# Performance work log

Measured on AMD Instinct MI355X. Metric: run time of the kernel, lower is better.

The kernel has to match this reference:

```python
import jax, jax.numpy as jnp
import numpy as np

EPS = 1e-8


def _cdist(a, b):
    # a: [B,N,3], b: [B,M,3] -> euclidean distances [B,N,M]
    a2 = jnp.sum(a * a, axis=-1)[:, :, None]          # [B,N,1]
    b2 = jnp.sum(b * b, axis=-1)[:, None, :]          # [B,1,M]
    ab = jnp.einsum('bnd,bmd->bnm', a, b)             # [B,N,M]
    d2 = jnp.maximum(a2 + b2 - 2.0 * ab, 0.0)
    return jnp.sqrt(d2)


def setup_inputs() -> dict:
    key = jax.random.key(0)
    ks = jax.random.split(key, 8)
    B, N, M, C1, C2 = 16, 4096, 1024, 128, 256
    Cin = C1 + C2  # 384
    H1, H2 = 256, 128
    return {
        'xyz1': jax.random.normal(ks[0], (B, N, 3), dtype=jnp.float32),
        'xyz2': jax.random.normal(ks[1], (B, M, 3), dtype=jnp.float32),
        'points1': jax.random.normal(ks[2], (B, C1, N), dtype=jnp.float32),
        'points2': jax.random.normal(ks[3], (B, C2, M), dtype=jnp.float32),
        'W1': jax.random.normal(ks[4], (H1, Cin), dtype=jnp.float32) * (1.0 / np.sqrt(Cin)),
        'b1': jnp.zeros((H1,), dtype=jnp.float32),
        'W2': jax.random.normal(ks[5], (H2, H1), dtype=jnp.float32) * (1.0 / np.sqrt(H1)),
        'b2': jnp.zeros((H2,), dtype=jnp.float32),
    }


def reference(xyz1, xyz2, points1, points2, W1, b1, W2, b2):
    # inverse-distance weighted interpolation over ALL M source points
    dist = _cdist(xyz1, xyz2) + EPS                   # [B,N,M]
    inv = 1.0 / dist
    weight = inv / jnp.sum(inv, axis=-1, keepdims=True)
    # interpolated features: [B,N,M] @ [B,M,C2] -> [B,C2,N]
    interpolated = jnp.einsum('bnm,bcm->bcn', weight, points2)
    new_points = jnp.concatenate([points1, interpolated], axis=1)  # [B,C1+C2,N]
    # 1x1 Conv1d MLP with ReLU
    h = jax.nn.relu(jnp.einsum('oc,bcn->bon', W1, new_points) + b1[None, :, None])
    out = jax.nn.relu(jnp.einsum('oc,bcn->bon', W2, h) + b2[None, :, None])
    return out
```

## Files before the change

kernel.cpp:

```cpp
#include <hip/hip_runtime.h>
#include <math.h>

#define BBATCH 16
#define NPTS   4096
#define MPTS   1024
#define C1c    128
#define C2c    256
#define CINc   384
#define H1c    256
#define H2c    128
#define TN     64

typedef _Float16 f16x8 __attribute__((ext_vector_type(8)));
typedef _Float16 f16x4 __attribute__((ext_vector_type(4)));
typedef float    f32x4 __attribute__((ext_vector_type(4)));

#define LDIW 136
#define LDXc 408
#define LDH  264

#define OFF_XYZ2  0
#define OFF_INV   12288
#define OFF_RED   47104
#define OFF_RECIP 52224
#define SMEM_BYTES 52480

#define NFRAG_P2  (BBATCH * 32 * 16 * 64)
#define NFRAG_W1  (16 * 12 * 64)
#define NFRAG_W2  (8 * 8 * 64)
#define WS_P2S  0
#define WS_W1S  (NFRAG_P2 * 8)
#define WS_W2S  (WS_W1S + NFRAG_W1 * 8)
#define WS_F16_TOTAL (WS_W2S + NFRAG_W2 * 8)

__global__ __launch_bounds__(256) void cvt_swz(
    const float* __restrict__ p2, const float* __restrict__ W1,
    const float* __restrict__ W2, _Float16* __restrict__ ws)
{
    const int t = blockIdx.x * 256 + threadIdx.x;
    const float* src;
    _Float16* dst;
    if (t < NFRAG_P2) {
        const int lane = t & 63, wt = (t >> 6) & 15, s = (t >> 10) & 31, b = t >> 15;
        const int c = wt * 16 + (lane & 15);
        const int m = s * 32 + (lane >> 4) * 8;
        src = p2 + ((size_t)(b * C2c + c)) * MPTS + m;
        dst = ws + WS_P2S + (size_t)t * 8;
    } else if (t < NFRAG_P2 + NFRAG_W1) {
        const int u = t - NFRAG_P2;
        const int lane = u & 63, kc = (u >> 6) % 12, wt = (u >> 6) / 12;
        const int o = wt * 16 + (lane & 15);
        const int k = kc * 32 + (lane >> 4) * 8;
        src = W1 + (size_t)o * CINc + k;
        dst = ws + WS_W1S + (size_t)u * 8;
    } else {
        const int v = t - NFRAG_P2 - NFRAG_W1;
        const int lane = v & 63, oc = (v >> 6) & 7, wt2 = v >> 9;
        const int o = wt2 * 16 + (lane & 15);
        const int k = oc * 32 + (lane >> 4) * 8;
        src = W2 + (size_t)o * H1c + k;
        dst = ws + WS_W2S + (size_t)v * 8;
    }
    const float4 a0 = *(const float4*)(src);
    const float4 a1 = *(const float4*)(src + 4);
    f16x8 h;
    h[0] = (_Float16)a0.x; h[1] = (_Float16)a0.y; h[2] = (_Float16)a0.z; h[3] = (_Float16)a0.w;
    h[4] = (_Float16)a1.x; h[5] = (_Float16)a1.y; h[6] = (_Float16)a1.z; h[7] = (_Float16)a1.w;
    *(f16x8*)dst = h;
}

template <bool F16P>
__global__ __launch_bounds__(256, 3) void fp_mfma7(
    const float* __restrict__ xyz1, const float* __restrict__ xyz2,
    const float* __restrict__ p1,   const float* __restrict__ p2,
    const float* __restrict__ W1,   const float* __restrict__ b1v,
    const float* __restrict__ W2,   const float* __restrict__ b2v,
    const _Float16* __restrict__ p2s, const _Float16* __restrict__ W1s,
    const _Float16* __restrict__ W2s,
    float* __restrict__ out)
{
    __shared__ __align__(16) char smem[SMEM_BYTES];
    float*    s_xyz2  = (float*)(smem + OFF_XYZ2);
    _Float16* s_inv   = (_Float16*)(smem + OFF_INV);
    float*    s_red   = (float*)(smem + OFF_RED);
    float*    s_recip = (float*)(smem + OFF_RECIP);
    _Float16* s_X     = (_Float16*)smem;
    _Float16* s_H     = (_Float16*)smem;

    const int tid  = threadIdx.x;
    const int w    = tid >> 6;
    const int L    = tid & 63;
    const int quad = L >> 4;
    const int l16  = L & 15;

    const int id = blockIdx.x;
    const int b  = (id & 7) * 2 + ((id >> 3) & 1);
    const int n0 = (id >> 4) * TN;

    const float* __restrict__ z2b = xyz2 + (size_t)b * MPTS * 3;
    const float* __restrict__ p2b = p2   + (size_t)b * C2c * MPTS;
    const _Float16* __restrict__ p2sb =
        F16P ? (p2s + (((size_t)b * 32 * 16 + (size_t)w * 4) * 64 + L) * 8) : (const _Float16*)nullptr;

    for (int i = tid; i < MPTS * 3 / 4; i += 256)
        ((f32x4*)s_xyz2)[i] = ((const f32x4*)z2b)[i];

    const float x1x = xyz1[((size_t)b * NPTS + n0 + L) * 3 + 0];
    const float x1y = xyz1[((size_t)b * NPTS + n0 + L) * 3 + 1];
    const float x1z = xyz1[((size_t)b * NPTS + n0 + L) * 3 + 2];

    f32x4 acc[4][4];
    #pragma unroll
    for (int ct = 0; ct < 4; ++ct)
        #pragma unroll
        for (int nt = 0; nt < 4; ++nt)
            acc[ct][nt] = (f32x4){0.f, 0.f, 0.f, 0.f};

    float ssum = 0.f;
    f16x8 Aa[2][4];

    auto loadA = [&](int s, f16x8 dst[4]) {
        if (F16P) {
            const _Float16* ap = p2sb + (size_t)s * (16 * 64 * 8);
            #pragma unroll
            for (int ct = 0; ct < 4; ++ct)
                dst[ct] = *(const f16x8*)(ap + (size_t)ct * (64 * 8));
        } else {
            const float* ap = p2b + (size_t)(w * 64 + l16) * MPTS + s * 32 + quad * 8;
            #pragma unroll
            for (int ct = 0; ct < 4; ++ct) {
                const float4 a0 = *(const float4*)(ap + (size_t)ct * (16 * MPTS));
                const float4 a1 = *(const float4*)(ap + (size_t)ct * (16 * MPTS) + 4);
                f16x8 h;
                h[0] = (_Float16)a0.x; h[1] = (_Float16)a0.y; h[2] = (_Float16)a0.z; h[3] = (_Float16)a0.w;
                h[4] = (_Float16)a1.x; h[5] = (_Float16)a1.y; h[6] = (_Float16)a1.z; h[7] = (_Float16)a1.w;
                dst[ct] = h;
            }
        }
    };

    auto gen = [&](int ss_) {
        _Float16* buf = s_inv + (ss_ & 1) * (64 * LDIW);
        #pragma unroll
        for (int g = 0; g < 4; ++g) {
            const float* zp = s_xyz2 + (size_t)(ss_ * 128 + w * 32 + g * 8) * 3;
            f32x4 zr[6];
            #pragma unroll
            for (int j = 0; j < 6; ++j) zr[j] = ((const f32x4*)zp)[j];
            const float* zv = (const float*)zr;
            f16x8 iv;
            #pragma unroll
            for (int i = 0; i < 8; ++i) {
                const float dx = x1x - zv[3 * i + 0];
                const float dy = x1y - zv[3 * i + 1];
                const float dz = x1z - zv[3 * i + 2];
                const float d2 = fmaf(dx, dx, fmaf(dy, dy, fmaf(dz, dz, 1e-12f)));
                const float inv = __builtin_amdgcn_rsqf(d2);
                ssum += inv;
                iv[i] = (_Float16)inv;
            }
            *(f16x8*)(buf + L * LDIW + w * 32 + g * 8) = iv;
        }
    };

    __syncthreads();
    loadA(0, Aa[0]);
    gen(0);
    __syncthreads();

    for (int ss = 0; ss < 8; ++ss) {
        if (ss + 1 < 8) gen(ss + 1);
        const _Float16* buf = s_inv + (ss & 1) * (64 * LDIW);
        #pragma unroll
        for (int cc = 0; cc < 4; ++cc) {
            const int s = ss * 4 + cc;
            if (s + 1 < 32) loadA(s + 1, Aa[(cc + 1) & 1]);
            const _Float16* bb = buf + l16 * LDIW + cc * 32 + quad * 8;
            #pragma unroll
            for (int nt = 0; nt < 4; ++nt) {
                const f16x8 bf = *(const f16x8*)(bb + nt * (16 * LDIW));
                #pragma unroll
                for (int ct = 0; ct < 4; ++ct)
                    acc[ct][nt] = __builtin_amdgcn_mfma_f32_16x16x32_f16(Aa[cc & 1][ct], bf, acc[ct][nt], 0, 0, 0);
            }
        }
        __syncthreads();
    }

    s_red[tid] = ssum;
    __syncthreads();
    if (tid < 64)
        s_recip[tid] = 1.0f / (s_red[tid] + s_red[tid + 64] + s_red[tid + 128] + s_red[tid + 192]);
    __syncthreads();

    {
        float rn4[4];
        #pragma unroll
        for (int nt = 0; nt < 4; ++nt) rn4[nt] = s_recip[nt * 16 + l16];
        #pragma unroll
        for (int ct = 0; ct < 4; ++ct)
            #pragma unroll
            for (int nt = 0; nt < 4; ++nt) {
                const f32x4 v = acc[ct][nt];
                const float r = rn4[nt];
                f16x4 hv;
                hv[0] = (_Float16)(v[0] * r);
                hv[1] = (_Float16)(v[1] * r);
                hv[2] = (_Float16)(v[2] * r);
                hv[3] = (_Float16)(v[3] * r);
                *(f16x4*)(&s_X[(nt * 16 + l16) * LDXc + 128 + w * 64 + ct * 16 + quad * 4]) = hv;
            }
    }
    {
        const float* p1b = p1 + (size_t)b * C1c * NPTS + n0;
        #pragma unroll
        for (int cc = 0; cc < 8; ++cc) {
            const int c = w * 32 + cc * 4;
            f16x4 v;
            v[0] = (_Float16)p1b[(size_t)(c + 0) * NPTS + L];
            v[1] = (_Float16)p1b[(size_t)(c + 1) * NPTS + L];
            v[2] = (_Float16)p1b[(size_t)(c + 2) * NPTS + L];
            v[3] = (_Float16)p1b[(size_t)(c + 3) * NPTS + L];
            *(f16x4*)(&s_X[L * LDXc + c]) = v;
        }
    }
    __syncthreads();

    f32x4 hacc[4][4];
    #pragma unroll
    for (int ct = 0; ct < 4; ++ct)
        #pragma unroll
        for (int nt = 0; nt < 4; ++nt)
            hacc[ct][nt] = (f32x4){0.f, 0.f, 0.f, 0.f};

    #pragma unroll 2
    for (int kc = 0; kc < 12; ++kc) {
        f16x8 af[4];
        if (F16P) {
            const _Float16* wp = W1s + (((size_t)(w * 4) * 12 + kc) * 64 + L) * 8;
            #pragma unroll
            for (int ct = 0; ct < 4; ++ct)
                af[ct] = *(const f16x8*)(wp + (size_t)ct * (12 * 64 * 8));
        } else {
            const float* wp = W1 + (size_t)(w * 64 + l16) * CINc + kc * 32 + quad * 8;
            #pragma unroll
            for (int ct = 0; ct < 4; ++ct) {
                const float4 a0 = *(const float4*)(wp + ct * (16 * CINc));
                const float4 a1 = *(const float4*)(wp + ct * (16 * CINc) + 4);
                f16x8 h;
                h[0] = (_Float16)a0.x; h[1] = (_Float16)a0.y; h[2] = (_Float16)a0.z; h[3] = (_Float16)a0.w;
                h[4] = (_Float16)a1.x; h[5] = (_Float16)a1.y; h[6] = (_Float16)a1.z; h[7] = (_Float16)a1.w;
                af[ct] = h;
            }
        }
        #pragma unroll
        for (int nt = 0; nt < 4; ++nt) {
            const f16x8 bf = *(const f16x8*)(&s_X[(nt * 16 + l16) * LDXc + kc * 32 + quad * 8]);
            #pragma unroll
            for (int ct = 0; ct < 4; ++ct)
                hacc[ct][nt] = __builtin_amdgcn_mfma_f32_16x16x32_f16(af[ct], bf, hacc[ct][nt], 0, 0, 0);
        }
    }

    __syncthreads();

    {
        f32x4 bb[4];
        #pragma unroll
        for (int ct = 0; ct < 4; ++ct)
            bb[ct] = *(const f32x4*)(b1v + w * 64 + ct * 16 + quad * 4);
        #pragma unroll
        for (int ct = 0; ct < 4; ++ct)
            #pragma unroll
            for (int nt = 0; nt < 4; ++nt) {
                const f32x4 v = hacc[ct][nt];
                f16x4 hv;
                hv[0] = (_Float16)fmaxf(v[0] + bb[ct][0], 0.f);
                hv[1] = (_Float16)fmaxf(v[1] + bb[ct][1], 0.f);
                hv[2] = (_Float16)fmaxf(v[2] + bb[ct][2], 0.f);
                hv[3] = (_Float16)fmaxf(v[3] + bb[ct][3], 0.f);
                *(f16x4*)(&s_H[(nt * 16 + l16) * LDH + w * 64 + ct * 16 + quad * 4]) = hv;
            }
    }
    __syncthreads();

    f32x4 oacc[2][4];
    #pragma unroll
    for (int ct = 0; ct < 2; ++ct)
        #pragma unroll
        for (int nt = 0; nt < 4; ++nt)
            oacc[ct][nt] = (f32x4){0.f, 0.f, 0.f, 0.f};

    #pragma unroll 2
    for (int oc = 0; oc < 8; ++oc) {
        f16x8 af2[2];
        if (F16P) {
            const _Float16* wp = W2s + (((size_t)(w * 2) * 8 + oc) * 64 + L) * 8;
            #pragma unroll
            for (int ct = 0; ct < 2; ++ct)
                af2[ct] = *(const f16x8*)(wp + (size_t)ct * (8 * 64 * 8));
        } else {
            const float* wp = W2 + (size_t)(w * 32 + l16) * H1c + oc * 32 + quad * 8;
            #pragma unroll
            for (int ct = 0; ct < 2; ++ct) {
                const float4 a0 = *(const float4*)(wp + ct * (16 * H1c));
                const float4 a1 = *(const float4*)(wp + ct * (16 * H1c) + 4);
                f16x8 h;
                h[0] = (_Float16)a0.x; h[1] = (_Float16)a0.y; h[2] = (_Float16)a0.z; h[3] = (_Float16)a0.w;
                h[4] = (_Float16)a1.x; h[5] = (_Float16)a1.y; h[6] = (_Float16)a1.z; h[7] = (_Float16)a1.w;
                af2[ct] = h;
            }
        }
        #pragma unroll
        for (int nt = 0; nt < 4; ++nt) {
            const f16x8 bf = *(const f16x8*)(&s_H[(nt * 16 + l16) * LDH + oc * 32 + quad * 8]);
            #pragma unroll
            for (int ct = 0; ct < 2; ++ct)
                oacc[ct][nt] = __builtin_amdgcn_mfma_f32_16x16x32_f16(af2[ct], bf, oacc[ct][nt], 0, 0, 0);
        }
    }

    {
        f32x4 bb2[2];
        #pragma unroll
        for (int ct = 0; ct < 2; ++ct)
            bb2[ct] = *(const f32x4*)(b2v + w * 32 + ct * 16 + quad * 4);
        #pragma unroll
        for (int ct = 0; ct < 2; ++ct)
            #pragma unroll
            for (int nt = 0; nt < 4; ++nt) {
                float* op = out + ((size_t)b * H2c + w * 32 + ct * 16 + quad * 4) * NPTS
                                + n0 + nt * 16 + l16;
                #pragma unroll
                for (int j = 0; j < 4; ++j)
                    op[(size_t)j * NPTS] = fmaxf(oacc[ct][nt][j] + bb2[ct][j], 0.f);
            }
    }
}

extern "C" void kernel_launch(void* const* d_in, const int* in_sizes, int n_in,
                              void* d_out, int out_size, void* d_ws, size_t ws_size,
                              hipStream_t stream) {
    (void)in_sizes; (void)n_in; (void)out_size;
    const float* xyz1 = (const float*)d_in[0];
    const float* xyz2 = (const float*)d_in[1];
    const float* p1   = (const float*)d_in[2];
    const float* p2   = (const float*)d_in[3];
    const float* W1   = (const float*)d_in[4];
    const float* b1   = (const float*)d_in[5];
    const float* W2   = (const float*)d_in[6];
    const float* b2   = (const float*)d_in[7];
    float* out = (float*)d_out;

    dim3 grid(BBATCH * (NPTS / TN));
    dim3 block(256);
    if (ws_size >= (size_t)WS_F16_TOTAL * 2) {
        _Float16* ws = (_Float16*)d_ws;
        const int nswz = NFRAG_P2 + NFRAG_W1 + NFRAG_W2;
        cvt_swz<<<dim3(nswz / 256), dim3(256), 0, stream>>>(p2, W1, W2, ws);
        fp_mfma7<true><<<grid, block, 0, stream>>>(xyz1, xyz2, p1, p2, W1, b1, W2, b2,
                                                   ws + WS_P2S, ws + WS_W1S, ws + WS_W2S, out);
    } else {
        fp_mfma7<false><<<grid, block, 0, stream>>>(xyz1, xyz2, p1, p2, W1, b1, W2, b2,
                                                    nullptr, nullptr, nullptr, out);
    }
}
```

Measured before the change: 171.7 us.

## Shrink LDS footprint with fragment-swizzled layouts and stream points1 directly into MFMA

Drops the shared-memory copy of xyz2 and reads it from global or L1 inside the generator. The inverse-distance, X and H buffers switch from padded row-major to MFMA-fragment-ordered layouts, so a single 32KB union plus a small reduction area replaces the 52KB allocation. points1 is no longer staged in LDS; its first four K-chunks are loaded from global and fed straight into MFMAs, and launch bounds are raised from 3 to 4 blocks per SM. The goal is higher occupancy and fewer LDS bank conflicts, at the cost of repeated global reads of xyz2 and strided uncoalesced-ish points1 loads inside the MLP.

```diff
diff --git a/kernel.cpp b/kernel.cpp
--- a/kernel.cpp
+++ b/kernel.cpp
@@ -15,15 +15,9 @@
 typedef _Float16 f16x4 __attribute__((ext_vector_type(4)));
 typedef float    f32x4 __attribute__((ext_vector_type(4)));
 
-#define LDIW 136
-#define LDXc 408
-#define LDH  264
-
-#define OFF_XYZ2  0
-#define OFF_INV   12288
-#define OFF_RED   47104
-#define OFF_RECIP 52224
-#define SMEM_BYTES 52480
+#define INV_HALF   8192
+#define SMEM_UNION 32768
+#define SMEM_BYTES (SMEM_UNION + 1024)
 
 #define NFRAG_P2  (BBATCH * 32 * 16 * 64)
 #define NFRAG_W1  (16 * 12 * 64)
@@ -70,7 +64,7 @@
 }
 
 template <bool F16P>
-__global__ __launch_bounds__(256, 3) void fp_mfma7(
+__global__ __launch_bounds__(256, 4) void fp_mfma8(
     const float* __restrict__ xyz1, const float* __restrict__ xyz2,
     const float* __restrict__ p1,   const float* __restrict__ p2,
     const float* __restrict__ W1,   const float* __restrict__ b1v,
@@ -80,12 +74,10 @@
     float* __restrict__ out)
 {
     __shared__ __align__(16) char smem[SMEM_BYTES];
-    float*    s_xyz2  = (float*)(smem + OFF_XYZ2);
-    _Float16* s_inv   = (_Float16*)(smem + OFF_INV);
-    float*    s_red   = (float*)(smem + OFF_RED);
-    float*    s_recip = (float*)(smem + OFF_RECIP);
-    _Float16* s_X     = (_Float16*)smem;
-    _Float16* s_H     = (_Float16*)smem;
+    _Float16* s_inv = (_Float16*)smem;
+    _Float16* s_X   = (_Float16*)smem;
+    _Float16* s_H   = (_Float16*)smem;
+    float*    s_red = (float*)(smem + SMEM_UNION);
 
     const int tid  = threadIdx.x;
     const int w    = tid >> 6;
@@ -101,9 +93,6 @@
     const float* __restrict__ p2b = p2   + (size_t)b * C2c * MPTS;
     const _Float16* __restrict__ p2sb =
         F16P ? (p2s + (((size_t)b * 32 * 16 + (size_t)w * 4) * 64 + L) * 8) : (const _Float16*)nullptr;
-
-    for (int i = tid; i < MPTS * 3 / 4; i += 256)
-        ((f32x4*)s_xyz2)[i] = ((const f32x4*)z2b)[i];
 
     const float x1x = xyz1[((size_t)b * NPTS + n0 + L) * 3 + 0];
     const float x1y = xyz1[((size_t)b * NPTS + n0 + L) * 3 + 1];
@@ -140,10 +129,11 @@
     };
 
     auto gen = [&](int ss_) {
-        _Float16* buf = s_inv + (ss_ & 1) * (64 * LDIW);
+        _Float16* buf = s_inv + (ss_ & 1) * INV_HALF;
+        const float* zbase = z2b + (size_t)(ss_ * 128 + w * 32) * 3;
         #pragma unroll
         for (int g = 0; g < 4; ++g) {
-            const float* zp = s_xyz2 + (size_t)(ss_ * 128 + w * 32 + g * 8) * 3;
+            const float* zp = zbase + g * 24;
             f32x4 zr[6];
             #pragma unroll
             for (int j = 0; j < 6; ++j) zr[j] = ((const f32x4*)zp)[j];
@@ -159,26 +149,24 @@
                 ssum += inv;
                 iv[i] = (_Float16)inv;
             }
-            *(f16x8*)(buf + L * LDIW + w * 32 + g * 8) = iv;
+            *(f16x8*)(buf + (((w * 4 + quad) * 64) + g * 16 + l16) * 8) = iv;
         }
     };
 
-    __syncthreads();
     loadA(0, Aa[0]);
     gen(0);
     __syncthreads();
 
     for (int ss = 0; ss < 8; ++ss) {
         if (ss + 1 < 8) gen(ss + 1);
-        const _Float16* buf = s_inv + (ss & 1) * (64 * LDIW);
+        const _Float16* buf = s_inv + (ss & 1) * INV_HALF;
         #pragma unroll
         for (int cc = 0; cc < 4; ++cc) {
             const int s = ss * 4 + cc;
             if (s + 1 < 32) loadA(s + 1, Aa[(cc + 1) & 1]);
-            const _Float16* bb = buf + l16 * LDIW + cc * 32 + quad * 8;
-            #pragma unroll
-            for (int nt = 0; nt < 4; ++nt) {
-                const f16x8 bf = *(const f16x8*)(bb + nt * (16 * LDIW));
+            #pragma unroll
+            for (int nt = 0; nt < 4; ++nt) {
+                const f16x8 bf = *(const f16x8*)(buf + ((cc * 4 + nt) * 64 + L) * 8);
                 #pragma unroll
                 for (int ct = 0; ct < 4; ++ct)
                     acc[ct][nt] = __builtin_amdgcn_mfma_f32_16x16x32_f16(Aa[cc & 1][ct], bf, acc[ct][nt], 0, 0, 0);
@@ -190,15 +178,18 @@
     s_red[tid] = ssum;
     __syncthreads();
     if (tid < 64)
-        s_recip[tid] = 1.0f / (s_red[tid] + s_red[tid + 64] + s_red[tid + 128] + s_red[tid + 192]);
+        s_red[tid] = 1.0f / (s_red[tid] + s_red[tid + 64] + s_red[tid + 128] + s_red[tid + 192]);
     __syncthreads();
 
     {
         float rn4[4];
         #pragma unroll
-        for (int nt = 0; nt < 4; ++nt) rn4[nt] = s_recip[nt * 16 + l16];
-        #pragma unroll
-        for (int ct = 0; ct < 4; ++ct)
+        for (int nt = 0; nt < 4; ++nt) rn4[nt] = s_red[nt * 16 + l16];
+        #pragma unroll
+        for (int ct = 0; ct < 4; ++ct) {
+            const int kq = 2 * w + (ct >> 1);
+            const int lp = l16 + 16 * (((ct & 1) * 2) + (quad >> 1));
+            const int jo = (quad & 1) * 4;
             #pragma unroll
             for (int nt = 0; nt < 4; ++nt) {
                 const f32x4 v = acc[ct][nt];
@@ -208,20 +199,8 @@
                 hv[1] = (_Float16)(v[1] * r);
                 hv[2] = (_Float16)(v[2] * r);
                 hv[3] = (_Float16)(v[3] * r);
-                *(f16x4*)(&s_X[(nt * 16 + l16) * LDXc + 128 + w * 64 + ct * 16 + quad * 4]) = hv;
-            }
-    }
-    {
-        const float* p1b = p1 + (size_t)b * C1c * NPTS + n0;
-        #pragma unroll
-        for (int cc = 0; cc < 8; ++cc) {
-            const int c = w * 32 + cc * 4;
-            f16x4 v;
-            v[0] = (_Float16)p1b[(size_t)(c + 0) * NPTS + L];
-            v[1] = (_Float16)p1b[(size_t)(c + 1) * NPTS + L];
-            v[2] = (_Float16)p1b[(size_t)(c + 2) * NPTS + L];
-            v[3] = (_Float16)p1b[(size_t)(c + 3) * NPTS + L];
-            *(f16x4*)(&s_X[L * LDXc + c]) = v;
+                *(f16x4*)(s_X + ((kq * 4 + nt) * 64 + lp) * 8 + jo) = hv;
+            }
         }
     }
     __syncthreads();
@@ -233,8 +212,46 @@
         for (int nt = 0; nt < 4; ++nt)
             hacc[ct][nt] = (f32x4){0.f, 0.f, 0.f, 0.f};
 
+    {
+        const float* p1f = p1 + ((size_t)b * C1c + quad * 8) * NPTS + n0 + l16;
+        #pragma unroll
+        for (int kc = 0; kc < 4; ++kc) {
+            f16x8 af[4];
+            if (F16P) {
+                const _Float16* wp = W1s + (((size_t)(w * 4) * 12 + kc) * 64 + L) * 8;
+                #pragma unroll
+                for (int ct = 0; ct < 4; ++ct)
+                    af[ct] = *(const f16x8*)(wp + (size_t)ct * (12 * 64 * 8));
+            } else {
+                const float* wp = W1 + (size_t)(w * 64 + l16) * CINc + kc * 32 + quad * 8;
+                #pragma unroll
+                for (int ct = 0; ct < 4; ++ct) {
+                    const float4 a0 = *(const float4*)(wp + ct * (16 * CINc));
+                    const float4 a1 = *(const float4*)(wp + ct * (16 * CINc) + 4);
+                    f16x8 h;
+                    h[0] = (_Float16)a0.x; h[1] = (_Float16)a0.y; h[2] = (_Float16)a0.z; h[3] = (_Float16)a0.w;
+                    h[4] = (_Float16)a1.x; h[5] = (_Float16)a1.y; h[6] = (_Float16)a1.z; h[7] = (_Float16)a1.w;
+                    af[ct] = h;
+                }
+            }
+            #pragma unroll
+            for (int nt = 0; nt < 4; ++nt) {
+                const float* pp = p1f + (size_t)(kc * 32) * NPTS + nt * 16;
+                float t[8];
+                #pragma unroll
+                for (int j = 0; j < 8; ++j) t[j] = pp[(size_t)j * NPTS];
+                f16x8 bf;
+                #pragma unroll
+                for (int j = 0; j < 8; ++j) bf[j] = (_Float16)t[j];
+                #pragma unroll
+                for (int ct = 0; ct < 4; ++ct)
+                    hacc[ct][nt] = __builtin_amdgcn_mfma_f32_16x16x32_f16(af[ct], bf, hacc[ct][nt], 0, 0, 0);
+            }
+        }
+    }
+
     #pragma unroll 2
-    for (int kc = 0; kc < 12; ++kc) {
+    for (int kc = 4; kc < 12; ++kc) {
         f16x8 af[4];
         if (F16P) {
             const _Float16* wp = W1s + (((size_t)(w * 4) * 12 + kc) * 64 + L) * 8;
@@ -255,7 +272,7 @@
         }
         #pragma unroll
         for (int nt = 0; nt < 4; ++nt) {
-            const f16x8 bf = *(const f16x8*)(&s_X[(nt * 16 + l16) * LDXc + kc * 32 + quad * 8]);
+            const f16x8 bf = *(const f16x8*)(s_X + (((kc - 4) * 4 + nt) * 64 + L) * 8);
             #pragma unroll
             for (int ct = 0; ct < 4; ++ct)
                 hacc[ct][nt] = __builtin_amdgcn_mfma_f32_16x16x32_f16(af[ct], bf, hacc[ct][nt], 0, 0, 0);
@@ -270,7 +287,10 @@
         for (int ct = 0; ct < 4; ++ct)
             bb[ct] = *(const f32x4*)(b1v + w * 64 + ct * 16 + quad * 4);
         #pragma unroll
-        for (int ct = 0; ct < 4; ++ct)
+        for (int ct = 0; ct < 4; ++ct) {
+            const int oq = 2 * w + (ct >> 1);
+            const int lp = l16 + 16 * (((ct & 1) * 2) + (quad >> 1));
+            const int jo = (quad & 1) * 4;
             #pragma unroll
             for (int nt = 0; nt < 4; ++nt) {
                 const f32x4 v = hacc[ct][nt];
@@ -279,8 +299,9 @@
                 hv[1] = (_Float16)fmaxf(v[1] + bb[ct][1], 0.f);
                 hv[2] = (_Float16)fmaxf(v[2] + bb[ct][2], 0.f);
                 hv[3] = (_Float16)fmaxf(v[3] + bb[ct][3], 0.f);
-                *(f16x4*)(&s_H[(nt * 16 + l16) * LDH + w * 64 + ct * 16 + quad * 4]) = hv;
-            }
+                *(f16x4*)(s_H + ((oq * 4 + nt) * 64 + lp) * 8 + jo) = hv;
+            }
+        }
     }
     __syncthreads();
 
@@ -313,7 +334,7 @@
         }
         #pragma unroll
         for (int nt = 0; nt < 4; ++nt) {
-            const f16x8 bf = *(const f16x8*)(&s_H[(nt * 16 + l16) * LDH + oc * 32 + quad * 8]);
+            const f16x8 bf = *(const f16x8*)(s_H + ((oc * 4 + nt) * 64 + L) * 8);
             #pragma unroll
             for (int ct = 0; ct < 2; ++ct)
                 oacc[ct][nt] = __builtin_amdgcn_mfma_f32_16x16x32_f16(af2[ct], bf, oacc[ct][nt], 0, 0, 0);
@@ -358,10 +379,10 @@
         _Float16* ws = (_Float16*)d_ws;
         const int nswz = NFRAG_P2 + NFRAG_W1 + NFRAG_W2;
         cvt_swz<<<dim3(nswz / 256), dim3(256), 0, stream>>>(p2, W1, W2, ws);
-        fp_mfma7<true><<<grid, block, 0, stream>>>(xyz1, xyz2, p1, p2, W1, b1, W2, b2,
+        fp_mfma8<true><<<grid, block, 0, stream>>>(xyz1, xyz2, p1, p2, W1, b1, W2, b2,
                                                    ws + WS_P2S, ws + WS_W1S, ws + WS_W2S, out);
     } else {
-        fp_mfma7<false><<<grid, block, 0, stream>>>(xyz1, xyz2, p1, p2, W1, b1, W2, b2,
+        fp_mfma8<false><<<grid, block, 0, stream>>>(xyz1, xyz2, p1, p2, W1, b1, W2, b2,
                                                     nullptr, nullptr, nullptr, out);
     }
 }
```

Result: slower. 186.3 us (+8.5%).
